# Optimization experiments

Hardware: AMD Instinct MI355X
Metric: run time of the kernel (lower is better)

## Reference

```python
import jax, jax.numpy as jnp
import numpy as np

N = 50000       # nodes
E = 800000      # edges (avg degree 16)
C_IN = 128
C_OUT = 128
H = 4           # attention heads
D = C_OUT // H  # per-head dim
G = 8           # group-norm groups
NEG_SLOPE_ACT = 0.01   # nn.LeakyReLU() default
NEG_SLOPE_ATT = 0.2    # GAT attention LeakyReLU slope


def _glorot(key, shape):
    fan = shape[0] + (shape[-1] if len(shape) > 1 else shape[0])
    lim = np.sqrt(6.0 / fan).astype(np.float32)
    return jax.random.uniform(key, shape, jnp.float32, -lim, lim)


def setup_inputs() -> dict:
    key = jax.random.key(0)
    ks = jax.random.split(key, 8)
    inp = {
        "x": jax.random.normal(ks[0], (N, C_IN), jnp.float32),
        "edge_index": jax.random.randint(ks[1], (2, E), 0, N),
        "edge_weight": jax.random.uniform(ks[2], (E,), jnp.float32),
    }
    dims = [C_IN, C_OUT]
    for l in range(2):
        cin = dims[l]
        k = jax.random.split(ks[3 + l], 8)
        inp[f"gamma{l}"] = jnp.ones((cin,), jnp.float32)
        inp[f"beta{l}"] = jnp.zeros((cin,), jnp.float32)
        inp[f"W{l}"] = _glorot(k[0], (cin, H * D))
        inp[f"We{l}"] = _glorot(k[1], (1, H * D))
        inp[f"a_src{l}"] = _glorot(k[2], (H, D))
        inp[f"a_dst{l}"] = _glorot(k[3], (H, D))
        inp[f"a_edge{l}"] = _glorot(k[4], (H, D))
        inp[f"bias{l}"] = jnp.zeros((H * D,), jnp.float32)
    return inp


def group_norm(x, gamma, beta, eps=1e-5):
    n, c = x.shape
    xg = x.reshape(n, G, c // G)
    mu = xg.mean(-1, keepdims=True)
    var = xg.var(-1, keepdims=True)
    xn = ((xg - mu) * jax.lax.rsqrt(var + eps)).reshape(n, c)
    return xn * gamma + beta


def gat_layer(x, src, dst, ew, W, We, a_src, a_dst, a_edge, bias):
    h = (x @ W).reshape(N, H, D)                   # [N,H,D]
    he = (ew[:, None] @ We).reshape(-1, H, D)      # [E',H,D] edge-weight embedding
    logits = ((h * a_src).sum(-1)[src]
              + (h * a_dst).sum(-1)[dst]
              + (he * a_edge).sum(-1))             # [E',H]
    logits = jax.nn.leaky_relu(logits, NEG_SLOPE_ATT)
    m = jax.ops.segment_max(logits, dst, num_segments=N)
    m = jax.lax.stop_gradient(jnp.where(jnp.isfinite(m), m, 0.0))
    e = jnp.exp(logits - m[dst])
    s = jax.ops.segment_sum(e, dst, num_segments=N)
    alpha = e / (s[dst] + 1e-16)                   # softmax over in-edges per dst, per head
    out = jax.ops.segment_sum(alpha[:, :, None] * h[src], dst, num_segments=N)
    return out.reshape(N, H * D) + bias


def reference(x, edge_index, edge_weight,
              gamma0, beta0, W0, We0, a_src0, a_dst0, a_edge0, bias0,
              gamma1, beta1, W1, We1, a_src1, a_dst1, a_edge1, bias1):
    loop = jnp.arange(N)
    src = jnp.concatenate([edge_index[0], loop])
    dst = jnp.concatenate([edge_index[1], loop])
    # self-loop fill_value='max': self edges get the max edge weight
    ew = jnp.concatenate([edge_weight, jnp.full((N,), edge_weight.max())])
    params = [(gamma0, beta0, W0, We0, a_src0, a_dst0, a_edge0, bias0),
              (gamma1, beta1, W1, We1, a_src1, a_dst1, a_edge1, bias1)]
    for g, b, W, We, asrc, adst, ae, bias in params:
        x = group_norm(x, g, b)
        x = jax.nn.leaky_relu(x, NEG_SLOPE_ACT)
        x = gat_layer(x, src, dst, ew, W, We, asrc, adst, ae, bias)
    return x
```

## Files before the change

kernel.cpp:

```cpp
#include <hip/hip_runtime.h>
#include <hip/hip_bf16.h>
#include <math.h>

#define CN 128
#define NBLK 256
#define BSH 8
#define CAPSH 13

typedef __attribute__((ext_vector_type(8))) short bf16x8;
typedef __attribute__((ext_vector_type(4))) float f32x4;

static __device__ inline unsigned int pack_bf16x2(float lo, float hi) {
    unsigned int ul = __float_as_uint(lo);
    unsigned int uh = __float_as_uint(hi);
    ul = (ul + 0x7fffu + ((ul >> 16) & 1u)) >> 16;
    uh = (uh + 0x7fffu + ((uh >> 16) & 1u)) & 0xffff0000u;
    return ul | uh;
}
static __device__ inline unsigned short bf16_of(float v) {
    unsigned int u = __float_as_uint(v);
    return (unsigned short)((u + 0x7fffu + ((u >> 16) & 1u)) >> 16);
}

__global__ __launch_bounds__(256) void kprep(const int* __restrict__ srcs,
                                             const int* __restrict__ dsts,
                                             const float* __restrict__ ew,
                                             int e, int n,
                                             int* __restrict__ cursors,
                                             int* __restrict__ ewmaxArr,
                                             int2* __restrict__ inter,
                                             const float* __restrict__ W0,
                                             const float* __restrict__ W1,
                                             const float* __restrict__ We0,
                                             const float* __restrict__ ae0,
                                             const float* __restrict__ We1,
                                             const float* __restrict__ ae1,
                                             unsigned short* __restrict__ wt0,
                                             unsigned short* __restrict__ wt1,
                                             float* __restrict__ ce) {
    __shared__ int lh[256];
    __shared__ int cur[256];
    __shared__ int wm[4];
    int t = threadIdx.x, blk = blockIdx.x;
    if (blk >= NBLK) {
        int b = blk - NBLK;
        if (b < 2) {
            const float* W = b ? W1 : W0;
            unsigned short* wt = b ? wt1 : wt0;
            for (int i = t; i < CN * CN; i += 256) {
                int k = i >> 7, c = i & 127;
                wt[c * CN + k] = bf16_of(W[k * CN + c]);
            }
        } else if (t < 8) {
            const float* We = (t < 4) ? We0 : We1;
            const float* ae = (t < 4) ? ae0 : ae1;
            int h = t & 3;
            float s = 0.f;
            for (int d = 0; d < 32; d++) s += We[h * 32 + d] * ae[h * 32 + d];
            ce[t] = s;
        }
        return;
    }
    lh[t] = 0;
    __syncthreads();
    int tot = e + n;
    int chunk = (tot + NBLK - 1) / NBLK;
    int start = blk * chunk, end = min(start + chunk, tot);
    float m = 0.f;
    for (int i = start + t; i < end; i += 256) {
        int d;
        if (i < e) { d = dsts[i]; m = fmaxf(m, ew[i]); }
        else       { d = i - e; }
        atomicAdd(&lh[d >> BSH], 1);
    }
#pragma unroll
    for (int off = 1; off < 64; off <<= 1) m = fmaxf(m, __shfl_xor(m, off));
    if ((t & 63) == 0) wm[t >> 6] = __float_as_int(m);
    __syncthreads();
    int c = lh[t];
    cur[t] = c ? atomicAdd(&cursors[t * 16], c) : 0;
    if (t == 0)
        ewmaxArr[blk] = max(max(wm[0], wm[1]), max(wm[2], wm[3]));
    __syncthreads();
    for (int i = start + t; i < end; i += 256) {
        int sn, d, wbits;
        if (i < e) { sn = srcs[i]; d = dsts[i]; wbits = __float_as_int(ew[i]); }
        else       { sn = i - e;   d = sn;      wbits = -1; }
        int b = d >> BSH;
        int p = atomicAdd(&cur[b], 1);
        inter[((size_t)b << CAPSH) + p] = make_int2((d << 16) | sn, wbits);
    }
}

static __device__ void kbc_body(int* cnt, int* cur, int* wsum, int* bexc,
                                int* wmI, int b,
                                const int* __restrict__ cursors,
                                const int* __restrict__ ewmaxArr,
                                const int2* __restrict__ inter,
                                unsigned int* __restrict__ edges,
                                int* __restrict__ rowptr,
                                int n, int nb, int ep) {
    int t = threadIdx.x;
    int lane = t & 63, wid = t >> 6;
    if (t == 0) *wmI = 0;
    int v = cursors[t * 16];
    int s = v;
#pragma unroll
    for (int off = 1; off < 64; off <<= 1) {
        int u = __shfl_up(s, off);
        if (lane >= off) s += u;
    }
    int mi = ewmaxArr[t];
#pragma unroll
    for (int off = 1; off < 64; off <<= 1) mi = max(mi, __shfl_xor(mi, off));
    if (lane == 63) wsum[wid] = s;
    __syncthreads();
    if (lane == 0) atomicMax(wmI, mi);
    int add = 0;
#pragma unroll
    for (int w = 0; w < 4; w++) if (w < wid) add += wsum[w];
    s += add;
    bexc[t] = s - v;
    if (t == 255) bexc[256] = s;
    cnt[t] = 0;
    __syncthreads();
    float wmax = __int_as_float(*wmI);
    int cntb = cursors[b * 16];
    size_t istart = (size_t)b << CAPSH;
    int gbase = bexc[b];
    for (int i = t; i < cntb; i += 256)
        atomicAdd(&cnt[(inter[istart + i].x >> 16) & 255], 1);
    __syncthreads();
    int v2 = cnt[t];
    int s2 = v2;
#pragma unroll
    for (int off = 1; off < 64; off <<= 1) {
        int u = __shfl_up(s2, off);
        if (lane >= off) s2 += u;
    }
    if (lane == 63) wsum[wid] = s2;
    __syncthreads();
    int wexcl = 0;
#pragma unroll
    for (int w = 0; w < 4; w++) if (w < wid) wexcl += wsum[w];
    int excl = wexcl + s2 - v2;
    int node = (b << BSH) + t;
    int gpos = gbase + excl;
    if (node < n) rowptr[node] = gpos;
    if (b == nb - 1 && t == 0) rowptr[n] = ep;
    cur[t] = gpos;
    __syncthreads();
    for (int i = t; i < cntb; i += 256) {
        int2 r = inter[istart + i];
        int p = atomicAdd(&cur[(r.x >> 16) & 255], 1);
        float w = (r.y == -1) ? wmax : __int_as_float(r.y);
        edges[p] = (unsigned int)(r.x & 0xffff) | ((unsigned int)bf16_of(w) << 16);
    }
}

static __device__ void kgn_body(short* xs, int block_row,
                                const float* __restrict__ xin,
                                const uint4* __restrict__ xin_b,
                                int inbf16, const float* __restrict__ gamma,
                                const float* __restrict__ beta,
                                const unsigned short* __restrict__ wt,
                                const float* __restrict__ asrc,
                                const float* __restrict__ adst,
                                unsigned int* __restrict__ hout,
                                float* __restrict__ ssrc,
                                float* __restrict__ sdst, int n) {
    int t = threadIdx.x;
    int lane = t & 63, w = t >> 6;
    int m = lane & 15, quad = lane >> 4;

    {
        int r = t & 63;
        int row = block_row + r;
        uint4* dst = (uint4*)xs;
#pragma unroll
        for (int u2 = 0; u2 < 2; u2++) {
            int g = (t >> 6) * 2 + u2;
            uint4 lo, hi;
            if (row < n) {
                float v[16];
                if (inbf16) {
                    uint4 A = xin_b[(size_t)row * 16 + g * 2];
                    uint4 B = xin_b[(size_t)row * 16 + g * 2 + 1];
                    unsigned int uu[8] = {A.x,A.y,A.z,A.w,B.x,B.y,B.z,B.w};
#pragma unroll
                    for (int j = 0; j < 8; j++) {
                        v[2*j]   = __uint_as_float(uu[j] << 16);
                        v[2*j+1] = __uint_as_float(uu[j] & 0xffff0000u);
                    }
                } else {
                    const float4* xr = (const float4*)(xin + (size_t)row * CN + g * 16);
                    float4 A = xr[0], B = xr[1], C = xr[2], D = xr[3];
                    float tmp[16] = {A.x,A.y,A.z,A.w,B.x,B.y,B.z,B.w,
                                     C.x,C.y,C.z,C.w,D.x,D.y,D.z,D.w};
#pragma unroll
                    for (int j = 0; j < 16; j++) v[j] = tmp[j];
                }
                float mu = 0.f;
#pragma unroll
                for (int j = 0; j < 16; j++) mu += v[j];
                mu *= 0.0625f;
                float var = 0.f;
#pragma unroll
                for (int j = 0; j < 16; j++) { float d2 = v[j] - mu; var += d2 * d2; }
                var *= 0.0625f;
                float rsv = rsqrtf(var + 1e-5f);
                const float4* gp = (const float4*)(gamma + g * 16);
                const float4* bp = (const float4*)(beta + g * 16);
                float4 g0 = gp[0], g1 = gp[1], g2 = gp[2], g3 = gp[3];
                float4 b0 = bp[0], b1 = bp[1], b2 = bp[2], b3 = bp[3];
                float gv[16] = {g0.x,g0.y,g0.z,g0.w,g1.x,g1.y,g1.z,g1.w,
                                g2.x,g2.y,g2.z,g2.w,g3.x,g3.y,g3.z,g3.w};
                float bv[16] = {b0.x,b0.y,b0.z,b0.w,b1.x,b1.y,b1.z,b1.w,
                                b2.x,b2.y,b2.z,b2.w,b3.x,b3.y,b3.z,b3.w};
                float xn[16];
#pragma unroll
                for (int j = 0; j < 16; j++) {
                    float xv = (v[j] - mu) * rsv * gv[j] + bv[j];
                    xn[j] = xv > 0.f ? xv : 0.01f * xv;
                }
                lo = make_uint4(pack_bf16x2(xn[0], xn[1]),  pack_bf16x2(xn[2], xn[3]),
                                pack_bf16x2(xn[4], xn[5]),  pack_bf16x2(xn[6], xn[7]));
                hi = make_uint4(pack_bf16x2(xn[8], xn[9]),  pack_bf16x2(xn[10], xn[11]),
                                pack_bf16x2(xn[12], xn[13]), pack_bf16x2(xn[14], xn[15]));
            } else {
                lo = make_uint4(0, 0, 0, 0);
                hi = lo;
            }
            dst[r * 16 + ((2 * g)     ^ (r & 15))] = lo;
            dst[r * 16 + ((2 * g + 1) ^ (r & 15))] = hi;
        }
    }
    __syncthreads();

    f32x4 acc[4][2];
#pragma unroll
    for (int i = 0; i < 4; i++) { acc[i][0] = (f32x4)0.f; acc[i][1] = (f32x4)0.f; }

#pragma unroll
    for (int kc = 0; kc < 4; kc++) {
        int kb = 4 * kc + quad;
        bf16x8 af[4], bfr[2];
#pragma unroll
        for (int mt = 0; mt < 4; mt++)
            af[mt] = *(const bf16x8*)&xs[(16 * mt + m) * CN + ((kb ^ m) << 3)];
#pragma unroll
        for (int nt = 0; nt < 2; nt++) {
            int c = 32 * w + 16 * nt + m;
            bfr[nt] = *(const bf16x8*)&wt[c * CN + (kb << 3)];
        }
#pragma unroll
        for (int mt = 0; mt < 4; mt++) {
#pragma unroll
            for (int nt = 0; nt < 2; nt++)
                acc[mt][nt] = __builtin_amdgcn_mfma_f32_16x16x32_bf16(
                    af[mt], bfr[nt], acc[mt][nt], 0, 0, 0);
        }
    }

    float asv[2], adv[2];
#pragma unroll
    for (int nt = 0; nt < 2; nt++) {
        asv[nt] = asrc[32 * w + 16 * nt + m];
        adv[nt] = adst[32 * w + 16 * nt + m];
    }
#pragma unroll
    for (int mt = 0; mt < 4; mt++) {
#pragma unroll
        for (int j = 0; j < 4; j++) {
            float p = acc[mt][0][j] * asv[0] + acc[mt][1][j] * asv[1];
            float q = acc[mt][0][j] * adv[0] + acc[mt][1][j] * adv[1];
#pragma unroll
            for (int off = 1; off < 16; off <<= 1) {
                p += __shfl_xor(p, off);
                q += __shfl_xor(q, off);
            }
            if (m == 0) {
                int row = block_row + 16 * mt + 4 * quad + j;
                if (row < n) {
                    ssrc[row * 4 + w] = p;
                    sdst[row * 4 + w] = q;
                }
            }
        }
    }

    __syncthreads();
#pragma unroll
    for (int mt = 0; mt < 4; mt++) {
#pragma unroll
        for (int nt = 0; nt < 2; nt++) {
            int c = 32 * w + 16 * nt + m;
#pragma unroll
            for (int j = 0; j < 4; j++) {
                int rl = 16 * mt + 4 * quad + j;
                xs[rl * CN + c] = (short)bf16_of(acc[mt][nt][j]);
            }
        }
    }
    __syncthreads();
    {
        const uint4* src = (const uint4*)xs;
#pragma unroll
        for (int i = 0; i < 4; i++) {
            int u = t + 256 * i;
            int rl = u >> 4;
            int row = block_row + rl;
            if (row < n)
                *(uint4*)&hout[(size_t)row * 64 + ((u & 15) << 2)] = src[u];
        }
    }
}

__global__ __launch_bounds__(256, 4) void kbCgn(
        const int* __restrict__ cursors, const int* __restrict__ ewmaxArr,
        const int2* __restrict__ inter, unsigned int* __restrict__ edges,
        int* __restrict__ rowptr, int n, int nb, int ep,
        const float* __restrict__ xin, const float* __restrict__ gamma,
        const float* __restrict__ beta, const unsigned short* __restrict__ wt,
        const float* __restrict__ asrc, const float* __restrict__ adst,
        unsigned int* __restrict__ hout, float* __restrict__ ssrcO,
        float* __restrict__ sdstO) {
    __shared__ short xs[64 * CN];
    if ((int)blockIdx.x < nb) {
        int* cnt  = (int*)xs;
        int* cur  = (int*)(xs + 512);
        int* wsum = (int*)(xs + 1024);
        int* wmI  = (int*)(xs + 1040);
        int* bexc = (int*)(xs + 2048);
        kbc_body(cnt, cur, wsum, bexc, wmI, blockIdx.x,
                 cursors, ewmaxArr, inter, edges, rowptr, n, nb, ep);
        return;
    }
    kgn_body(xs, ((int)blockIdx.x - nb) * 64, xin, (const uint4*)0, 0,
             gamma, beta, wt, asrc, adst, hout, ssrcO, sdstO, n);
}

__global__ __launch_bounds__(256, 4) void kgn_gemm7(
        const float* __restrict__ xin, const uint4* __restrict__ xin_b,
        int inbf16, const float* __restrict__ gamma,
        const float* __restrict__ beta, const unsigned short* __restrict__ wt,
        const float* __restrict__ asrc, const float* __restrict__ adst,
        unsigned int* __restrict__ hout, float* __restrict__ ssrc,
        float* __restrict__ sdst, int n) {
    __shared__ short xs[64 * CN];
    kgn_body(xs, blockIdx.x * 64, xin, xin_b, inbf16,
             gamma, beta, wt, asrc, adst, hout, ssrc, sdst, n);
}

__global__ __launch_bounds__(256, 8) void kaggr3(
        const uint4* __restrict__ h, const float* __restrict__ ssrc,
        const float* __restrict__ sdst, const int* __restrict__ rowptr,
        const unsigned int* __restrict__ edges, const float* __restrict__ ce4,
        const float* __restrict__ bias, float* __restrict__ out,
        uint4* __restrict__ outb, int packout, int n) {
    int t = threadIdx.x;
    int node = blockIdx.x * 4 + (t >> 6);
    if (node >= n) return;
    int l64 = t & 63;
    int ll = l64 & 15;
    int g  = l64 >> 4;
    int head = ll >> 2;

    int start = rowptr[node], end = rowptr[node + 1];
    float sd = sdst[node * 4 + head];
    float ce = ce4[head];

    float a0=0.f,a1=0.f,a2=0.f,a3=0.f,a4=0.f,a5=0.f,a6=0.f,a7=0.f;
    float se = 0.f;

    int i = start + g;
    for (; i + 12 < end; i += 16) {
        unsigned int er[4];
#pragma unroll
        for (int u = 0; u < 4; u++) er[u] = edges[i + 4 * u];
        float ssv[4]; uint4 U[4];
#pragma unroll
        for (int u = 0; u < 4; u++) {
            int sidx = er[u] & 0xffff;
            ssv[u] = ssrc[sidx * 4 + head];
            U[u] = h[(size_t)sidx * 16 + ll];
        }
#pragma unroll
        for (int u = 0; u < 4; u++) {
            float wv = __uint_as_float(er[u] & 0xffff0000u);
            float l = ssv[u] + sd + wv * ce;
            l = fmaxf(l, 0.2f * l);
            float e = __expf(fminf(l, 80.f));
            float h0 = __uint_as_float(U[u].x << 16);
            float h1 = __uint_as_float(U[u].x & 0xffff0000u);
            float h2 = __uint_as_float(U[u].y << 16);
            float h3 = __uint_as_float(U[u].y & 0xffff0000u);
            float h4 = __uint_as_float(U[u].z << 16);
            float h5 = __uint_as_float(U[u].z & 0xffff0000u);
            float h6 = __uint_as_float(U[u].w << 16);
            float h7 = __uint_as_float(U[u].w & 0xffff0000u);
            se += e;
            a0 = fmaf(e, h0, a0); a1 = fmaf(e, h1, a1);
            a2 = fmaf(e, h2, a2); a3 = fmaf(e, h3, a3);
            a4 = fmaf(e, h4, a4); a5 = fmaf(e, h5, a5);
            a6 = fmaf(e, h6, a6); a7 = fmaf(e, h7, a7);
        }
    }
    for (; i < end; i += 4) {
        unsigned int er = edges[i];
        int sidx = er & 0xffff;
        float ss = ssrc[sidx * 4 + head];
        uint4 U = h[(size_t)sidx * 16 + ll];
        float wv = __uint_as_float(er & 0xffff0000u);
        float l = ss + sd + wv * ce;
        l = fmaxf(l, 0.2f * l);
        float e = __expf(fminf(l, 80.f));
        float h0 = __uint_as_float(U.x << 16);
        float h1 = __uint_as_float(U.x & 0xffff0000u);
        float h2 = __uint_as_float(U.y << 16);
        float h3 = __uint_as_float(U.y & 0xffff0000u);
        float h4 = __uint_as_float(U.z << 16);
        float h5 = __uint_as_float(U.z & 0xffff0000u);
        float h6 = __uint_as_float(U.w << 16);
        float h7 = __uint_as_float(U.w & 0xffff0000u);
        se += e;
        a0 = fmaf(e, h0, a0); a1 = fmaf(e, h1, a1);
        a2 = fmaf(e, h2, a2); a3 = fmaf(e, h3, a3);
        a4 = fmaf(e, h4, a4); a5 = fmaf(e, h5, a5);
        a6 = fmaf(e, h6, a6); a7 = fmaf(e, h7, a7);
    }
#pragma unroll
    for (int off = 16; off < 64; off <<= 1) {
        a0 += __shfl_xor(a0, off); a1 += __shfl_xor(a1, off);
        a2 += __shfl_xor(a2, off); a3 += __shfl_xor(a3, off);
        a4 += __shfl_xor(a4, off); a5 += __shfl_xor(a5, off);
        a6 += __shfl_xor(a6, off); a7 += __shfl_xor(a7, off);
        se += __shfl_xor(se, off);
    }
    if (g == 0) {
        float inv = 1.f / (se + 1e-16f);
        const float4* bp = (const float4*)(bias + ll * 8);
        float4 b0 = bp[0], b1 = bp[1];
        float o0 = a0 * inv + b0.x, o1 = a1 * inv + b0.y;
        float o2 = a2 * inv + b0.z, o3 = a3 * inv + b0.w;
        float o4 = a4 * inv + b1.x, o5 = a5 * inv + b1.y;
        float o6 = a6 * inv + b1.z, o7 = a7 * inv + b1.w;
        if (packout) {
            outb[(size_t)node * 16 + ll] =
                make_uint4(pack_bf16x2(o0, o1), pack_bf16x2(o2, o3),
                           pack_bf16x2(o4, o5), pack_bf16x2(o6, o7));
        } else {
            float4* orow = (float4*)(out + (size_t)node * CN + ll * 8);
            orow[0] = make_float4(o0, o1, o2, o3);
            orow[1] = make_float4(o4, o5, o6, o7);
        }
    }
}

extern "C" void kernel_launch(void* const* d_in, const int* in_sizes, int n_in,
                              void* d_out, int out_size, void* d_ws, size_t ws_size,
                              hipStream_t stream) {
    const float* x  = (const float*)d_in[0];
    const int*   ei = (const int*)d_in[1];
    const float* ew = (const float*)d_in[2];
    int N_ = in_sizes[0] / CN;
    int E_ = in_sizes[2];
    int EP = E_ + N_;
    int NB = (N_ + 255) >> BSH;
    int NT = (N_ + 63) / 64;

    size_t off = 0;
    auto alloc = [&](size_t bytes) -> void* {
        void* p = (char*)d_ws + off;
        off += (bytes + 255) & ~(size_t)255;
        return p;
    };
    unsigned int* hbuf = (unsigned int*)alloc((size_t)N_ * 64 * 4);
    uint4* x1b     = (uint4*)alloc((size_t)N_ * 64 * 4);
    float* ssrc    = (float*)alloc((size_t)N_ * 4 * 4);
    float* sdst    = (float*)alloc((size_t)N_ * 4 * 4);
    int*   rowptr  = (int*)alloc((size_t)(N_ + 1) * 4);
    unsigned int* edges = (unsigned int*)alloc((size_t)EP * 4);
    int2*  inter   = (int2*)alloc((size_t)256 << CAPSH << 3);
    int*   cursors = (int*)alloc((size_t)256 * 16 * 4);
    int*   ewmaxArr= (int*)alloc((size_t)NBLK * 4);
    unsigned short* wt0 = (unsigned short*)alloc((size_t)CN * CN * 2);
    unsigned short* wt1 = (unsigned short*)alloc((size_t)CN * CN * 2);
    float* cedge   = (float*)alloc(256);

    hipMemsetAsync(cursors, 0, (size_t)256 * 16 * 4, stream);

    const int* srcs = ei;
    const int* dsts = ei + E_;

    kprep<<<NBLK + 3, 256, 0, stream>>>(srcs, dsts, ew, E_, N_, cursors, ewmaxArr,
                                        inter,
                                        (const float*)d_in[5], (const float*)d_in[13],
                                        (const float*)d_in[6], (const float*)d_in[9],
                                        (const float*)d_in[14], (const float*)d_in[17],
                                        wt0, wt1, cedge);

    kbCgn<<<NB + NT, 256, 0, stream>>>(
        cursors, ewmaxArr, inter, edges, rowptr, N_, NB, EP,
        x, (const float*)d_in[3], (const float*)d_in[4], wt0,
        (const float*)d_in[7], (const float*)d_in[8],
        hbuf, ssrc, sdst);

    kaggr3<<<(N_ + 3) / 4, 256, 0, stream>>>(
        (const uint4*)hbuf, ssrc, sdst, rowptr, edges, cedge,
        (const float*)d_in[10], (float*)d_out, x1b, 1, N_);

    kgn_gemm7<<<NT, 256, 0, stream>>>(
        x, (const uint4*)x1b, 1, (const float*)d_in[11], (const float*)d_in[12],
        wt1, (const float*)d_in[15], (const float*)d_in[16],
        hbuf, ssrc, sdst, N_);
    kaggr3<<<(N_ + 3) / 4, 256, 0, stream>>>(
        (const uint4*)hbuf, ssrc, sdst, rowptr, edges, cedge + 4,
        (const float*)d_in[18], (float*)d_out, x1b, 0, N_);
}
```

Measured before the change: 247.1 us.

## Fuse layer-0 aggregation with layer-1 group-norm and GEMM in one kernel

Layer-0 edge aggregation, group norm, LeakyReLU, bf16 packing, the layer-1 MFMA GEMM and the attention-score projection now run in one kernel. Each block aggregates its 64 rows one wave per row into shared memory, then multiplies the tile by W1 in place. This removes a launch and the bf16 round-trip of the intermediate x1 through global memory. In exchange, aggregation parallelism drops from 4 nodes per block to 64 rows per block with serial per-wave loops, which may raise load imbalance and lower occupancy. Layer-1 outputs go to separate buffers so they do not overwrite the layer-0 inputs still being read.

```diff
diff --git a/kernel.cpp b/kernel.cpp
--- a/kernel.cpp
+++ b/kernel.cpp
@@ -160,8 +160,7 @@
 
 static __device__ void kgn_body(short* xs, int block_row,
                                 const float* __restrict__ xin,
-                                const uint4* __restrict__ xin_b,
-                                int inbf16, const float* __restrict__ gamma,
+                                const float* __restrict__ gamma,
                                 const float* __restrict__ beta,
                                 const unsigned short* __restrict__ wt,
                                 const float* __restrict__ asrc,
@@ -183,23 +182,12 @@
             uint4 lo, hi;
             if (row < n) {
                 float v[16];
-                if (inbf16) {
-                    uint4 A = xin_b[(size_t)row * 16 + g * 2];
-                    uint4 B = xin_b[(size_t)row * 16 + g * 2 + 1];
-                    unsigned int uu[8] = {A.x,A.y,A.z,A.w,B.x,B.y,B.z,B.w};
-#pragma unroll
-                    for (int j = 0; j < 8; j++) {
-                        v[2*j]   = __uint_as_float(uu[j] << 16);
-                        v[2*j+1] = __uint_as_float(uu[j] & 0xffff0000u);
-                    }
-                } else {
-                    const float4* xr = (const float4*)(xin + (size_t)row * CN + g * 16);
-                    float4 A = xr[0], B = xr[1], C = xr[2], D = xr[3];
-                    float tmp[16] = {A.x,A.y,A.z,A.w,B.x,B.y,B.z,B.w,
-                                     C.x,C.y,C.z,C.w,D.x,D.y,D.z,D.w};
-#pragma unroll
-                    for (int j = 0; j < 16; j++) v[j] = tmp[j];
-                }
+                const float4* xr = (const float4*)(xin + (size_t)row * CN + g * 16);
+                float4 A = xr[0], B = xr[1], C = xr[2], D = xr[3];
+                float tmp[16] = {A.x,A.y,A.z,A.w,B.x,B.y,B.z,B.w,
+                                 C.x,C.y,C.z,C.w,D.x,D.y,D.z,D.w};
+#pragma unroll
+                for (int j = 0; j < 16; j++) v[j] = tmp[j];
                 float mu = 0.f;
 #pragma unroll
                 for (int j = 0; j < 16; j++) mu += v[j];
@@ -336,28 +324,221 @@
                  cursors, ewmaxArr, inter, edges, rowptr, n, nb, ep);
         return;
     }
-    kgn_body(xs, ((int)blockIdx.x - nb) * 64, xin, (const uint4*)0, 0,
+    kgn_body(xs, ((int)blockIdx.x - nb) * 64, xin,
              gamma, beta, wt, asrc, adst, hout, ssrcO, sdstO, n);
 }
 
-__global__ __launch_bounds__(256, 4) void kgn_gemm7(
-        const float* __restrict__ xin, const uint4* __restrict__ xin_b,
-        int inbf16, const float* __restrict__ gamma,
-        const float* __restrict__ beta, const unsigned short* __restrict__ wt,
+__global__ __launch_bounds__(256, 6) void kfuse(
+        const uint4* __restrict__ h, const float* __restrict__ ssrc,
+        const float* __restrict__ sdst, const int* __restrict__ rowptr,
+        const unsigned int* __restrict__ edges, const float* __restrict__ ce4,
+        const float* __restrict__ bias0,
+        const float* __restrict__ gamma, const float* __restrict__ beta,
+        const unsigned short* __restrict__ wt,
         const float* __restrict__ asrc, const float* __restrict__ adst,
-        unsigned int* __restrict__ hout, float* __restrict__ ssrc,
-        float* __restrict__ sdst, int n) {
+        unsigned int* __restrict__ hout, float* __restrict__ ssrcO,
+        float* __restrict__ sdstO, int n) {
     __shared__ short xs[64 * CN];
-    kgn_body(xs, blockIdx.x * 64, xin, xin_b, inbf16,
-             gamma, beta, wt, asrc, adst, hout, ssrc, sdst, n);
+    int t = threadIdx.x;
+    int lane = t & 63, w = t >> 6;
+    int ll = lane & 15, g = lane >> 4;
+    int head = ll >> 2;
+    int block_row = blockIdx.x * 64;
+
+    for (int q = 0; q < 16; q++) {
+        int r = q * 4 + w;
+        int node = block_row + r;
+        float a0=0.f,a1=0.f,a2=0.f,a3=0.f,a4=0.f,a5=0.f,a6=0.f,a7=0.f;
+        float se = 0.f;
+        if (node < n) {
+            int start = rowptr[node], end = rowptr[node + 1];
+            float sd = sdst[node * 4 + head];
+            float ce = ce4[head];
+            int i = start + g;
+            for (; i + 12 < end; i += 16) {
+                unsigned int er[4];
+#pragma unroll
+                for (int u = 0; u < 4; u++) er[u] = edges[i + 4 * u];
+                float ssv[4]; uint4 U[4];
+#pragma unroll
+                for (int u = 0; u < 4; u++) {
+                    int sidx = er[u] & 0xffff;
+                    ssv[u] = ssrc[sidx * 4 + head];
+                    U[u] = h[(size_t)sidx * 16 + ll];
+                }
+#pragma unroll
+                for (int u = 0; u < 4; u++) {
+                    float wv = __uint_as_float(er[u] & 0xffff0000u);
+                    float l = ssv[u] + sd + wv * ce;
+                    l = fmaxf(l, 0.2f * l);
+                    float e = __expf(fminf(l, 80.f));
+                    float h0 = __uint_as_float(U[u].x << 16);
+                    float h1 = __uint_as_float(U[u].x & 0xffff0000u);
+                    float h2 = __uint_as_float(U[u].y << 16);
+                    float h3 = __uint_as_float(U[u].y & 0xffff0000u);
+                    float h4 = __uint_as_float(U[u].z << 16);
+                    float h5 = __uint_as_float(U[u].z & 0xffff0000u);
+                    float h6 = __uint_as_float(U[u].w << 16);
+                    float h7 = __uint_as_float(U[u].w & 0xffff0000u);
+                    se += e;
+                    a0 = fmaf(e, h0, a0); a1 = fmaf(e, h1, a1);
+                    a2 = fmaf(e, h2, a2); a3 = fmaf(e, h3, a3);
+                    a4 = fmaf(e, h4, a4); a5 = fmaf(e, h5, a5);
+                    a6 = fmaf(e, h6, a6); a7 = fmaf(e, h7, a7);
+                }
+            }
+            for (; i < end; i += 4) {
+                unsigned int er = edges[i];
+                int sidx = er & 0xffff;
+                float ss = ssrc[sidx * 4 + head];
+                uint4 U = h[(size_t)sidx * 16 + ll];
+                float wv = __uint_as_float(er & 0xffff0000u);
+                float l = ss + sd + wv * ce;
+                l = fmaxf(l, 0.2f * l);
+                float e = __expf(fminf(l, 80.f));
+                float h0 = __uint_as_float(U.x << 16);
+                float h1 = __uint_as_float(U.x & 0xffff0000u);
+                float h2 = __uint_as_float(U.y << 16);
+                float h3 = __uint_as_float(U.y & 0xffff0000u);
+                float h4 = __uint_as_float(U.z << 16);
+                float h5 = __uint_as_float(U.z & 0xffff0000u);
+                float h6 = __uint_as_float(U.w << 16);
+                float h7 = __uint_as_float(U.w & 0xffff0000u);
+                se += e;
+                a0 = fmaf(e, h0, a0); a1 = fmaf(e, h1, a1);
+                a2 = fmaf(e, h2, a2); a3 = fmaf(e, h3, a3);
+                a4 = fmaf(e, h4, a4); a5 = fmaf(e, h5, a5);
+                a6 = fmaf(e, h6, a6); a7 = fmaf(e, h7, a7);
+            }
+#pragma unroll
+            for (int off = 16; off < 64; off <<= 1) {
+                a0 += __shfl_xor(a0, off); a1 += __shfl_xor(a1, off);
+                a2 += __shfl_xor(a2, off); a3 += __shfl_xor(a3, off);
+                a4 += __shfl_xor(a4, off); a5 += __shfl_xor(a5, off);
+                a6 += __shfl_xor(a6, off); a7 += __shfl_xor(a7, off);
+                se += __shfl_xor(se, off);
+            }
+        }
+        if (g == 0) {
+            uint4 P = make_uint4(0, 0, 0, 0);
+            if (node < n) {
+                float inv = 1.f / (se + 1e-16f);
+                const float4* bp = (const float4*)(bias0 + ll * 8);
+                float4 bb0 = bp[0], bb1 = bp[1];
+                float o0 = a0 * inv + bb0.x, o1 = a1 * inv + bb0.y;
+                float o2 = a2 * inv + bb0.z, o3 = a3 * inv + bb0.w;
+                float o4 = a4 * inv + bb1.x, o5 = a5 * inv + bb1.y;
+                float o6 = a6 * inv + bb1.z, o7 = a7 * inv + bb1.w;
+                float ps = o0 + o1 + o2 + o3 + o4 + o5 + o6 + o7;
+                ps += __shfl_xor(ps, 1);
+                float mu = ps * 0.0625f;
+                float d0 = o0 - mu, d1 = o1 - mu, d2 = o2 - mu, d3 = o3 - mu;
+                float d4 = o4 - mu, d5 = o5 - mu, d6 = o6 - mu, d7 = o7 - mu;
+                float v2 = d0*d0 + d1*d1 + d2*d2 + d3*d3
+                         + d4*d4 + d5*d5 + d6*d6 + d7*d7;
+                v2 += __shfl_xor(v2, 1);
+                float rsv = rsqrtf(v2 * 0.0625f + 1e-5f);
+                const float4* gp = (const float4*)(gamma + ll * 8);
+                const float4* bq = (const float4*)(beta + ll * 8);
+                float4 g0 = gp[0], g1 = gp[1], be0 = bq[0], be1 = bq[1];
+                float x0 = d0 * rsv * g0.x + be0.x, x1 = d1 * rsv * g0.y + be0.y;
+                float x2 = d2 * rsv * g0.z + be0.z, x3 = d3 * rsv * g0.w + be0.w;
+                float x4 = d4 * rsv * g1.x + be1.x, x5 = d5 * rsv * g1.y + be1.y;
+                float x6 = d6 * rsv * g1.z + be1.z, x7 = d7 * rsv * g1.w + be1.w;
+                x0 = x0 > 0.f ? x0 : 0.01f * x0;  x1 = x1 > 0.f ? x1 : 0.01f * x1;
+                x2 = x2 > 0.f ? x2 : 0.01f * x2;  x3 = x3 > 0.f ? x3 : 0.01f * x3;
+                x4 = x4 > 0.f ? x4 : 0.01f * x4;  x5 = x5 > 0.f ? x5 : 0.01f * x5;
+                x6 = x6 > 0.f ? x6 : 0.01f * x6;  x7 = x7 > 0.f ? x7 : 0.01f * x7;
+                P = make_uint4(pack_bf16x2(x0, x1), pack_bf16x2(x2, x3),
+                               pack_bf16x2(x4, x5), pack_bf16x2(x6, x7));
+            }
+            ((uint4*)xs)[r * 16 + (ll ^ (r & 15))] = P;
+        }
+    }
+    __syncthreads();
+
+    int m = ll, quad = g;
+    f32x4 acc[4][2];
+#pragma unroll
+    for (int i = 0; i < 4; i++) { acc[i][0] = (f32x4)0.f; acc[i][1] = (f32x4)0.f; }
+#pragma unroll
+    for (int kc = 0; kc < 4; kc++) {
+        int kb = 4 * kc + quad;
+        bf16x8 af[4], bfr[2];
+#pragma unroll
+        for (int mt = 0; mt < 4; mt++)
+            af[mt] = *(const bf16x8*)&xs[(16 * mt + m) * CN + ((kb ^ m) << 3)];
+#pragma unroll
+        for (int nt = 0; nt < 2; nt++) {
+            int c = 32 * w + 16 * nt + m;
+            bfr[nt] = *(const bf16x8*)&wt[c * CN + (kb << 3)];
+        }
+#pragma unroll
+        for (int mt = 0; mt < 4; mt++) {
+#pragma unroll
+            for (int nt = 0; nt < 2; nt++)
+                acc[mt][nt] = __builtin_amdgcn_mfma_f32_16x16x32_bf16(
+                    af[mt], bfr[nt], acc[mt][nt], 0, 0, 0);
+        }
+    }
+    float asv[2], adv[2];
+#pragma unroll
+    for (int nt = 0; nt < 2; nt++) {
+        asv[nt] = asrc[32 * w + 16 * nt + m];
+        adv[nt] = adst[32 * w + 16 * nt + m];
+    }
+#pragma unroll
+    for (int mt = 0; mt < 4; mt++) {
+#pragma unroll
+        for (int j = 0; j < 4; j++) {
+            float p = acc[mt][0][j] * asv[0] + acc[mt][1][j] * asv[1];
+            float q2 = acc[mt][0][j] * adv[0] + acc[mt][1][j] * adv[1];
+#pragma unroll
+            for (int off = 1; off < 16; off <<= 1) {
+                p += __shfl_xor(p, off);
+                q2 += __shfl_xor(q2, off);
+            }
+            if (m == 0) {
+                int row = block_row + 16 * mt + 4 * quad + j;
+                if (row < n) {
+                    ssrcO[row * 4 + w] = p;
+                    sdstO[row * 4 + w] = q2;
+                }
+            }
+        }
+    }
+    __syncthreads();
+#pragma unroll
+    for (int mt = 0; mt < 4; mt++) {
+#pragma unroll
+        for (int nt = 0; nt < 2; nt++) {
+            int c = 32 * w + 16 * nt + m;
+#pragma unroll
+            for (int j = 0; j < 4; j++) {
+                int rl = 16 * mt + 4 * quad + j;
+                xs[rl * CN + c] = (short)bf16_of(acc[mt][nt][j]);
+            }
+        }
+    }
+    __syncthreads();
+    {
+        const uint4* src = (const uint4*)xs;
+#pragma unroll
+        for (int i = 0; i < 4; i++) {
+            int u = t + 256 * i;
+            int rl = u >> 4;
+            int row = block_row + rl;
+            if (row < n)
+                *(uint4*)&hout[(size_t)row * 64 + ((u & 15) << 2)] = src[u];
+        }
+    }
 }
 
 __global__ __launch_bounds__(256, 8) void kaggr3(
         const uint4* __restrict__ h, const float* __restrict__ ssrc,
         const float* __restrict__ sdst, const int* __restrict__ rowptr,
         const unsigned int* __restrict__ edges, const float* __restrict__ ce4,
-        const float* __restrict__ bias, float* __restrict__ out,
-        uint4* __restrict__ outb, int packout, int n) {
+        const float* __restrict__ bias, float* __restrict__ out, int n) {
     int t = threadIdx.x;
     int node = blockIdx.x * 4 + (t >> 6);
     if (node >= n) return;
@@ -445,15 +626,9 @@
         float o2 = a2 * inv + b0.z, o3 = a3 * inv + b0.w;
         float o4 = a4 * inv + b1.x, o5 = a5 * inv + b1.y;
         float o6 = a6 * inv + b1.z, o7 = a7 * inv + b1.w;
-        if (packout) {
-            outb[(size_t)node * 16 + ll] =
-                make_uint4(pack_bf16x2(o0, o1), pack_bf16x2(o2, o3),
-                           pack_bf16x2(o4, o5), pack_bf16x2(o6, o7));
-        } else {
-            float4* orow = (float4*)(out + (size_t)node * CN + ll * 8);
-            orow[0] = make_float4(o0, o1, o2, o3);
-            orow[1] = make_float4(o4, o5, o6, o7);
-        }
+        float4* orow = (float4*)(out + (size_t)node * CN + ll * 8);
+        orow[0] = make_float4(o0, o1, o2, o3);
+        orow[1] = make_float4(o4, o5, o6, o7);
     }
 }
 
@@ -475,10 +650,12 @@
         off += (bytes + 255) & ~(size_t)255;
         return p;
     };
-    unsigned int* hbuf = (unsigned int*)alloc((size_t)N_ * 64 * 4);
-    uint4* x1b     = (uint4*)alloc((size_t)N_ * 64 * 4);
+    unsigned int* hbuf  = (unsigned int*)alloc((size_t)N_ * 64 * 4);
+    unsigned int* hbuf2 = (unsigned int*)alloc((size_t)N_ * 64 * 4);
     float* ssrc    = (float*)alloc((size_t)N_ * 4 * 4);
     float* sdst    = (float*)alloc((size_t)N_ * 4 * 4);
+    float* ssrc2   = (float*)alloc((size_t)N_ * 4 * 4);
+    float* sdst2   = (float*)alloc((size_t)N_ * 4 * 4);
     int*   rowptr  = (int*)alloc((size_t)(N_ + 1) * 4);
     unsigned int* edges = (unsigned int*)alloc((size_t)EP * 4);
     int2*  inter   = (int2*)alloc((size_t)256 << CAPSH << 3);
@@ -506,15 +683,14 @@
         (const float*)d_in[7], (const float*)d_in[8],
         hbuf, ssrc, sdst);
 
+    kfuse<<<NT, 256, 0, stream>>>(
+        (const uint4*)hbuf, ssrc, sdst, rowptr, edges, cedge,
+        (const float*)d_in[10],
+        (const float*)d_in[11], (const float*)d_in[12], wt1,
+        (const float*)d_in[15], (const float*)d_in[16],
+        hbuf2, ssrc2, sdst2, N_);
+
     kaggr3<<<(N_ + 3) / 4, 256, 0, stream>>>(
-        (const uint4*)hbuf, ssrc, sdst, rowptr, edges, cedge,
-        (const float*)d_in[10], (float*)d_out, x1b, 1, N_);
-
-    kgn_gemm7<<<NT, 256, 0, stream>>>(
-        x, (const uint4*)x1b, 1, (const float*)d_in[11], (const float*)d_in[12],
-        wt1, (const float*)d_in[15], (const float*)d_in[16],
-        hbuf, ssrc, sdst, N_);
-    kaggr3<<<(N_ + 3) / 4, 256, 0, stream>>>(
-        (const uint4*)hbuf, ssrc, sdst, rowptr, edges, cedge + 4,
-        (const float*)d_in[18], (float*)d_out, x1b, 0, N_);
-}
+        (const uint4*)hbuf2, ssrc2, sdst2, rowptr, edges, cedge + 4,
+        (const float*)d_in[18], (float*)d_out, N_);
+}
```

After: 255.8 us. +3.5%, slower.
